# Kernel optimization log

Hardware: AMD Instinct MI355X
Metric: run time of the kernel (lower is better)

The kernel has to match this reference:

```python
import jax, jax.numpy as jnp
import numpy as np

N_NODES = 50000
IN_C = 128
OUT_C = 128
N_EDGES = 1600000
NEG_SLOPE = 0.2
EPS = 1e-16  # matches torch_geometric softmax denominator epsilon


def setup_inputs() -> dict:
    key = jax.random.key(0)
    k1, k2, k3, k4, k5 = jax.random.split(key, 5)
    glorot = 1.0 / np.sqrt(IN_C)
    x = jax.random.normal(k1, (N_NODES, IN_C), dtype=jnp.float32)
    W = jax.random.normal(k2, (IN_C, OUT_C), dtype=jnp.float32) * glorot
    a_src = jax.random.normal(k3, (OUT_C,), dtype=jnp.float32) * glorot
    a_dst = jax.random.normal(k4, (OUT_C,), dtype=jnp.float32) * glorot
    bias = jnp.zeros((OUT_C,), dtype=jnp.float32)
    edge_index = jax.random.randint(k5, (2, N_EDGES), 0, N_NODES, dtype=jnp.int32)
    return {"x": x, "W": W, "a_src": a_src, "a_dst": a_dst,
            "bias": bias, "edge_index": edge_index}


def reference(x, W, a_src, a_dst, bias, edge_index):
    N = x.shape[0]
    # add self loops (GATConv default add_self_loops=True)
    loops = jnp.arange(N, dtype=edge_index.dtype)
    src = jnp.concatenate([edge_index[0], loops])  # [E+N]
    dst = jnp.concatenate([edge_index[1], loops])

    h = x @ W                                      # [N, out]
    alpha_s = h @ a_src                            # [N]
    alpha_d = h @ a_dst                            # [N]

    e = alpha_s[src] + alpha_d[dst]                # [E+N]
    e = jnp.where(e > 0, e, NEG_SLOPE * e)         # leaky_relu

    # neighbor-wise (per destination node) stable softmax
    m = jax.ops.segment_max(e, dst, num_segments=N)
    ex = jnp.exp(e - m[dst])
    denom = jax.ops.segment_sum(ex, dst, num_segments=N)
    alpha = ex / (denom[dst] + EPS)

    # weighted aggregation of source features into destination nodes
    msgs = h[src] * alpha[:, None]                 # [E+N, out]
    out = jax.ops.segment_sum(msgs, dst, num_segments=N) + bias
    return jax.nn.relu(out)
```

## Files before the change

kernel.cpp:

```cpp
#include <hip/hip_runtime.h>
#include <hip/hip_fp16.h>

#define C 128
#define NEG_SLOPE 0.2f
#define SM_EPS 1e-16f
#define BKT_SHIFT 8
#define BKT_MASK 255
#define BIN_CHUNK 8192
#define WP 136

typedef unsigned int uint32;
typedef __attribute__((ext_vector_type(8))) short bf16x8;
typedef __attribute__((ext_vector_type(4))) float f32x4;

static __device__ __forceinline__ unsigned short f2bf(float f) {
    uint32 u = __float_as_uint(f);
    uint32 r = 0x7FFFu + ((u >> 16) & 1u);
    return (unsigned short)((u + r) >> 16);
}
static __device__ __forceinline__ uint32 f2bf2(float lo, float hi) {
    return (uint32)f2bf(lo) | ((uint32)f2bf(hi) << 16);
}
static __device__ __forceinline__ uint32 f2h(float f) {
    __half h = __float2half(f);
    return (uint32)*reinterpret_cast<unsigned short*>(&h);
}
static __device__ __forceinline__ float h2f(uint32 b) {
    unsigned short s = (unsigned short)(b & 0xffffu);
    __half h = *reinterpret_cast<__half*>(&s);
    return __half2float(h);
}

__global__ __launch_bounds__(256) void cvtw_kernel(const float* __restrict__ W,
                                                   uint32* __restrict__ Wf,
                                                   int* __restrict__ bucket_cnt,
                                                   int* __restrict__ bucket_progress, int NB) {
    int gid = blockIdx.x * 256 + threadIdx.x;
    if (blockIdx.x == 0 && threadIdx.x < NB) {
        bucket_cnt[threadIdx.x] = 0;
        bucket_progress[threadIdx.x] = 0;
    }
    int j2   = gid & 3;
    int lane = (gid >> 2) & 63;
    int tile = gid >> 8;
    int t = tile >> 2, kk = tile & 3;
    int n = t * 16 + (lane & 15);
    int k = kk * 32 + (lane >> 4) * 8 + j2 * 2;
    Wf[gid] = f2bf2(W[k * C + n], W[(k + 1) * C + n]);
}

__global__ __launch_bounds__(256) void gemm_hist_kernel(
    const float* __restrict__ x, const uint32* __restrict__ Wf,
    const float* __restrict__ a_src, const float* __restrict__ a_dst,
    unsigned short* __restrict__ hb, float* __restrict__ as_out,
    float* __restrict__ ad_out, int N,
    const int* __restrict__ dst, int* __restrict__ bucket_cnt, int E, int total, int NB)
{
    __shared__ __align__(16) unsigned short slice[4][16 * WP];
    __shared__ int bhist[256];

    const int tid  = threadIdx.x;
    const int lane = tid & 63;
    const int w    = tid >> 6;
    const int row0 = blockIdx.x * 64;
    const int m16  = lane & 15;
    const int q    = lane >> 4;

    bhist[tid] = 0;

    const int row = row0 + w * 16 + m16;
    const bool rv = (row < N);
    const float* xr_p = x + (size_t)(rv ? row : 0) * C + q * 8;

    float4 xr[8];
    #pragma unroll
    for (int kk = 0; kk < 4; ++kk) {
        xr[kk * 2]     = rv ? *(const float4*)(xr_p + kk * 32)     : make_float4(0, 0, 0, 0);
        xr[kk * 2 + 1] = rv ? *(const float4*)(xr_p + kk * 32 + 4) : make_float4(0, 0, 0, 0);
    }

    f32x4 acc[8];
    const f32x4 zz = {0.f, 0.f, 0.f, 0.f};
    #pragma unroll
    for (int t = 0; t < 8; ++t) acc[t] = zz;

    #pragma unroll
    for (int kk = 0; kk < 4; ++kk) {
        union { bf16x8 v; uint32 u[4]; } au;
        float4 p0 = xr[kk * 2], p1 = xr[kk * 2 + 1];
        au.u[0] = f2bf2(p0.x, p0.y); au.u[1] = f2bf2(p0.z, p0.w);
        au.u[2] = f2bf2(p1.x, p1.y); au.u[3] = f2bf2(p1.z, p1.w);
        #pragma unroll
        for (int t = 0; t < 8; ++t) {
            bf16x8 b = *(const bf16x8*)&Wf[((t * 4 + kk) * 64 + lane) * 4];
            acc[t] = __builtin_amdgcn_mfma_f32_16x16x32_bf16(au.v, b, acc[t], 0, 0, 0);
        }
    }

    float ps[4] = {0.f, 0.f, 0.f, 0.f}, pd[4] = {0.f, 0.f, 0.f, 0.f};
    #pragma unroll
    for (int t = 0; t < 8; ++t) {
        float av = a_src[t * 16 + m16];
        float dv = a_dst[t * 16 + m16];
        #pragma unroll
        for (int r = 0; r < 4; ++r) {
            ps[r] += acc[t][r] * av;
            pd[r] += acc[t][r] * dv;
        }
    }
    #pragma unroll
    for (int r = 0; r < 4; ++r) {
        #pragma unroll
        for (int off = 1; off < 16; off <<= 1) {
            ps[r] += __shfl_xor(ps[r], off, 64);
            pd[r] += __shfl_xor(pd[r], off, 64);
        }
    }
    if (m16 == 0) {
        #pragma unroll
        for (int r = 0; r < 4; ++r) {
            int rr = row0 + w * 16 + q * 4 + r;
            if (rr < N) { as_out[rr] = ps[r]; ad_out[rr] = pd[r]; }
        }
    }

    #pragma unroll
    for (int t = 0; t < 8; ++t)
        #pragma unroll
        for (int r = 0; r < 4; ++r)
            slice[w][(q * 4 + r) * WP + t * 16 + m16] = f2bf(acc[t][r]);
    __syncthreads();
    #pragma unroll
    for (int it = 0; it < 4; ++it) {
        int r = it * 4 + q;
        int rr = row0 + w * 16 + r;
        if (rr < N) {
            bf16x8 v = *(const bf16x8*)&slice[w][r * WP + m16 * 8];
            *(bf16x8*)&hb[(size_t)rr * C + m16 * 8] = v;
        }
    }

    for (int i = blockIdx.x * 256 + tid; i < total; i += gridDim.x * 256) {
        int d = (i < E) ? dst[i] : (i - E);
        atomicAdd(&bhist[d >> BKT_SHIFT], 1);
    }
    __syncthreads();
    if (tid < NB && bhist[tid]) atomicAdd(&bucket_cnt[tid], bhist[tid]);
}

__global__ __launch_bounds__(1024) void bin_kernel(
    const int* __restrict__ src, const int* __restrict__ dst,
    const int* __restrict__ bucket_cnt, int* __restrict__ bucket_progress,
    uint32* __restrict__ packed, int E, int total, int NB)
{
    __shared__ uint32 lsrc[BIN_CHUNK];
    __shared__ unsigned short ldst[BIN_CHUNK];
    __shared__ int hist[256];
    __shared__ int base[256];
    __shared__ int boff[256];
    __shared__ int wave_tot[4];
    const int tid = threadIdx.x;
    const int start = blockIdx.x * BIN_CHUNK;
    const int end = min(start + BIN_CHUNK, total);
    const int n = end - start;

    int v = 0, xx = 0;
    if (tid < 256) {
        hist[tid] = 0;
        const int lane = tid & 63;
        v = (tid < NB) ? bucket_cnt[tid] : 0;
        xx = v;
        #pragma unroll
        for (int o = 1; o < 64; o <<= 1) {
            int t = __shfl_up(xx, o, 64);
            if (lane >= o) xx += t;
        }
        if (lane == 63) wave_tot[tid >> 6] = xx;
    }
    for (int i = start + tid; i < end; i += 1024) {
        int s = (i < E) ? src[i] : (i - E);
        int d = (i < E) ? dst[i] : (i - E);
        lsrc[i - start] = (uint32)s;
        ldst[i - start] = (unsigned short)d;
    }
    __syncthreads();
    if (tid < 256) {
        const int wid = tid >> 6;
        int wbase = 0;
        #pragma unroll
        for (int w = 0; w < 4; ++w) wbase += (w < wid) ? wave_tot[w] : 0;
        boff[tid] = wbase + xx - v;
    }
    __syncthreads();
    for (int j = tid; j < n; j += 1024)
        atomicAdd(&hist[ldst[j] >> BKT_SHIFT], 1);
    __syncthreads();
    if (tid < NB) {
        int c = hist[tid];
        base[tid] = boff[tid] + (c ? atomicAdd(&bucket_progress[tid], c) : 0);
    }
    if (tid < 256) hist[tid] = 0;
    __syncthreads();
    for (int j = tid; j < n; j += 1024) {
        int d = ldst[j];
        int b = d >> BKT_SHIFT;
        int pos = base[b] + atomicAdd(&hist[b], 1);
        packed[pos] = (lsrc[j] << BKT_SHIFT) | (uint32)(d & BKT_MASK);
    }
}

__global__ __launch_bounds__(1024) void build_kernel(
    const uint32* __restrict__ packed, const int* __restrict__ bucket_cnt,
    const float* __restrict__ as, const float* __restrict__ ad,
    int* __restrict__ row_start, uint32* __restrict__ csr, int N, int NB, int total)
{
    __shared__ int cnt[256];
    __shared__ int cur[256];
    __shared__ float adl[256];
    __shared__ int boff[256];
    __shared__ int wave_tot[8];
    const int tid = threadIdx.x;
    const int b = blockIdx.x;

    int v = 0, xx = 0;
    if (tid < 256) {
        const int lane = tid & 63;
        v = (tid < NB) ? bucket_cnt[tid] : 0;
        xx = v;
        #pragma unroll
        for (int o = 1; o < 64; o <<= 1) {
            int t = __shfl_up(xx, o, 64);
            if (lane >= o) xx += t;
        }
        if (lane == 63) wave_tot[tid >> 6] = xx;
        cnt[tid] = 0;
        int g = (b << BKT_SHIFT) + tid;
        adl[tid] = (g < N) ? ad[g] : 0.f;
    }
    __syncthreads();
    if (tid < 256) {
        const int wid = tid >> 6;
        int wbase = 0;
        #pragma unroll
        for (int w = 0; w < 4; ++w) wbase += (w < wid) ? wave_tot[w] : 0;
        boff[tid] = wbase + xx - v;
    }
    __syncthreads();
    const int off = boff[b];
    const int end = off + ((b < NB) ? bucket_cnt[b] : 0);
    if (b == 0 && tid == 0) row_start[N] = total;

    for (int j = off + tid; j < end; j += 1024)
        atomicAdd(&cnt[packed[j] & BKT_MASK], 1);
    __syncthreads();

    int v2 = 0, x2 = 0;
    if (tid < 256) {
        const int lane = tid & 63;
        v2 = cnt[tid]; x2 = v2;
        #pragma unroll
        for (int o = 1; o < 64; o <<= 1) {
            int t = __shfl_up(x2, o, 64);
            if (lane >= o) x2 += t;
        }
        if (lane == 63) wave_tot[4 + (tid >> 6)] = x2;
    }
    __syncthreads();
    if (tid < 256) {
        const int wid = tid >> 6;
        int wbase = 0;
        #pragma unroll
        for (int w = 0; w < 4; ++w) wbase += (w < wid) ? wave_tot[4 + w] : 0;
        int excl = wbase + x2 - v2;
        int g = (b << BKT_SHIFT) + tid;
        if (g < N) row_start[g] = off + excl;
        cur[tid] = excl;
    }
    __syncthreads();

    for (int j = off + tid; j < end; j += 1024) {
        uint32 p = packed[j];
        int l = (int)(p & BKT_MASK);
        int s = (int)(p >> BKT_SHIFT);
        float e = as[s] + adl[l];
        e = (e > 0.f) ? e : NEG_SLOPE * e;
        int pos = atomicAdd(&cur[l], 1);
        csr[off + pos] = ((uint32)s << 16) | f2h(e);
    }
}

static __device__ __forceinline__ void gather_node_fw(
    int d, const uint32* __restrict__ csr, const int* __restrict__ row_start,
    const unsigned short* __restrict__ hb, const float* __restrict__ bias,
    float* __restrict__ out, int lane)
{
    const int beg = row_start[d];
    const int deg = row_start[d + 1] - beg;
    const int c2 = lane << 1;
    float a0 = 0.f, a1 = 0.f;
    float m = -INFINITY;
    for (int t = lane; t < deg; t += 64) m = fmaxf(m, h2f(csr[beg + t]));
    #pragma unroll
    for (int off = 32; off > 0; off >>= 1) m = fmaxf(m, __shfl_xor(m, off, 64));
    float ssum = 0.f;
    for (int t = lane; t < deg; t += 64) ssum += __expf(h2f(csr[beg + t]) - m);
    #pragma unroll
    for (int off = 32; off > 0; off >>= 1) ssum += __shfl_xor(ssum, off, 64);
    float inv = 1.f / (ssum + SM_EPS);
    for (int t0 = 0; t0 < deg; t0 += 64) {
        int nc = min(64, deg - t0);
        uint32 ent = (lane < nc) ? csr[beg + t0 + lane] : 0xFC00u;
        float wl = (lane < nc) ? __expf(h2f(ent) - m) * inv : 0.f;
        uint32 bc = (ent & 0xffff0000u) | f2h(wl);
        for (int t = 0; t < nc; ++t) {
            uint32 b0 = (uint32)__shfl((int)bc, t, 64);
            uint32 u0 = *(const uint32*)&hb[(size_t)(b0 >> 16) * C + c2];
            float w0 = h2f(b0);
            a0 += __uint_as_float(u0 << 16) * w0;
            a1 += __uint_as_float(u0 & 0xffff0000u) * w0;
        }
    }
    float2 b2 = *(const float2*)&bias[c2];
    a0 = fmaxf(a0 + b2.x, 0.f);
    a1 = fmaxf(a1 + b2.y, 0.f);
    *(float2*)&out[(size_t)d * C + c2] = make_float2(a0, a1);
}

#define ACC4(r, wgt)                                           \
    {                                                          \
        a0 += __uint_as_float((r).x << 16)         * (wgt);    \
        a1 += __uint_as_float((r).x & 0xffff0000u) * (wgt);    \
        a2 += __uint_as_float((r).y << 16)         * (wgt);    \
        a3 += __uint_as_float((r).y & 0xffff0000u) * (wgt);    \
    }

__global__ __launch_bounds__(256) void gather_kernel(
    const uint32* __restrict__ csr, const int* __restrict__ row_start,
    const unsigned short* __restrict__ hb, const float* __restrict__ bias,
    float* __restrict__ out, int N)
{
    __shared__ __align__(16) uint2 lent[4][2][64];
    const int w    = threadIdx.x >> 6;
    const int lane = threadIdx.x & 63;
    const int half = lane >> 5;
    const int hl   = lane & 31;
    const int pair = blockIdx.x * 4 + w;
    const int d0 = pair * 2;
    if (d0 >= N) return;
    const int d = d0 + half;
    const bool valid = (d < N);

    int beg = 0, deg = 0;
    if (valid) { beg = row_start[d]; deg = row_start[d + 1] - beg; }

    int wdeg = deg;
    #pragma unroll
    for (int off = 32; off > 0; off >>= 1) wdeg = max(wdeg, __shfl_xor(wdeg, off, 64));

    if (wdeg > 64) {
        gather_node_fw(d0, csr, row_start, hb, bias, out, lane);
        if (d0 + 1 < N) gather_node_fw(d0 + 1, csr, row_start, hb, bias, out, lane);
        return;
    }

    uint32 ent0 = (hl < deg) ? csr[beg + hl] : 0xFC00u;
    uint32 ent1 = (32 + hl < deg) ? csr[beg + 32 + hl] : 0xFC00u;
    float e0 = h2f(ent0), e1 = h2f(ent1);
    float m = fmaxf(e0, e1);
    #pragma unroll
    for (int off = 16; off > 0; off >>= 1) m = fmaxf(m, __shfl_xor(m, off, 64));
    float p0 = (hl < deg) ? __expf(e0 - m) : 0.f;
    float p1 = (32 + hl < deg) ? __expf(e1 - m) : 0.f;
    float ssum = p0 + p1;
    #pragma unroll
    for (int off = 16; off > 0; off >>= 1) ssum += __shfl_xor(ssum, off, 64);
    const float inv = 1.f / (ssum + SM_EPS);

    lent[w][half][hl]      = make_uint2((ent0 & 0xffff0000u) >> 8, __float_as_uint(p0 * inv));
    lent[w][half][32 + hl] = make_uint2((ent1 & 0xffff0000u) >> 8, __float_as_uint(p1 * inv));
    __builtin_amdgcn_wave_barrier();

    const uint32 cb = (uint32)(hl << 3);
    const char* hbB = (const char*)hb;
    const uint2* lp = &lent[w][half][0];
    float a0 = 0.f, a1 = 0.f, a2 = 0.f, a3 = 0.f;

    int t = 0;
    for (; t + 8 <= deg; t += 8) {
        uint4 q0 = *(const uint4*)(lp + t);
        uint4 q1 = *(const uint4*)(lp + t + 2);
        uint4 q2 = *(const uint4*)(lp + t + 4);
        uint4 q3 = *(const uint4*)(lp + t + 6);
        uint2 r0 = *(const uint2*)(hbB + (q0.x + cb));
        uint2 r1 = *(const uint2*)(hbB + (q0.z + cb));
        uint2 r2 = *(const uint2*)(hbB + (q1.x + cb));
        uint2 r3 = *(const uint2*)(hbB + (q1.z + cb));
        uint2 r4 = *(const uint2*)(hbB + (q2.x + cb));
        uint2 r5 = *(const uint2*)(hbB + (q2.z + cb));
        uint2 r6 = *(const uint2*)(hbB + (q3.x + cb));
        uint2 r7 = *(const uint2*)(hbB + (q3.z + cb));
        float w0 = __uint_as_float(q0.y), w1 = __uint_as_float(q0.w);
        float w2 = __uint_as_float(q1.y), w3 = __uint_as_float(q1.w);
        float w4 = __uint_as_float(q2.y), w5 = __uint_as_float(q2.w);
        float w6 = __uint_as_float(q3.y), w7 = __uint_as_float(q3.w);
        ACC4(r0, w0) ACC4(r1, w1) ACC4(r2, w2) ACC4(r3, w3)
        ACC4(r4, w4) ACC4(r5, w5) ACC4(r6, w6) ACC4(r7, w7)
    }
    for (; t < deg; ++t) {
        uint2 q = lp[t];
        uint2 r = *(const uint2*)(hbB + (q.x + cb));
        float wt = __uint_as_float(q.y);
        ACC4(r, wt)
    }

    if (valid) {
        const int c4 = hl << 2;
        float4 bb = *(const float4*)&bias[c4];
        float4 o;
        o.x = fmaxf(a0 + bb.x, 0.f);
        o.y = fmaxf(a1 + bb.y, 0.f);
        o.z = fmaxf(a2 + bb.z, 0.f);
        o.w = fmaxf(a3 + bb.w, 0.f);
        *(float4*)&out[(size_t)d * C + c4] = o;
    }
}

extern "C" void kernel_launch(void* const* d_in, const int* in_sizes, int n_in,
                              void* d_out, int out_size, void* d_ws, size_t ws_size,
                              hipStream_t stream) {
    const float* x     = (const float*)d_in[0];
    const float* W     = (const float*)d_in[1];
    const float* a_src = (const float*)d_in[2];
    const float* a_dst = (const float*)d_in[3];
    const float* bias  = (const float*)d_in[4];
    const int*   edge  = (const int*)d_in[5];

    const int N = in_sizes[0] / C;
    const int E = in_sizes[5] / 2;
    const int total = E + N;
    const int* src = edge;
    const int* dst = edge + E;
    float* out = (float*)d_out;

    const int NB = (N + BKT_MASK) >> BKT_SHIFT;

    float* ws = (float*)d_ws;
    unsigned short* hb = (unsigned short*)ws;
    float* as = (float*)(hb + (size_t)N * C);
    float* ad = as + N;
    int* row_start       = (int*)(ad + N);
    uint32* packed       = (uint32*)(row_start + (N + 2));
    uint32* csr          = packed + total;
    uint32* Wf           = csr + total;
    int* bucket_cnt      = (int*)(Wf + 8192);
    int* bucket_progress = bucket_cnt + NB;

    cvtw_kernel<<<32, 256, 0, stream>>>(W, Wf, bucket_cnt, bucket_progress, NB);
    gemm_hist_kernel<<<(N + 63) / 64, 256, 0, stream>>>(
        x, Wf, a_src, a_dst, hb, as, ad, N, dst, bucket_cnt, E, total, NB);
    bin_kernel<<<(total + BIN_CHUNK - 1) / BIN_CHUNK, 1024, 0, stream>>>(
        src, dst, bucket_cnt, bucket_progress, packed, E, total, NB);
    build_kernel<<<NB, 1024, 0, stream>>>(packed, bucket_cnt, as, ad, row_start,
                                          csr, N, NB, total);
    gather_kernel<<<((N + 1) / 2 + 3) / 4, 256, 0, stream>>>(csr, row_start, hb, bias, out, N);
}
```

Before: 203.8 us.

## Replace bucketed two-pass CSR build with per-node atomic count, scan, scatter

Drops the bucket histogram plus bin/build kernels in favour of a per-destination-node degree count done with global atomics in the GEMM kernel, a single-block prefix scan, and an atomic-position scatter that writes the CSR entries directly. This removes the intermediate packed buffer and one full pass over the edges. The costs are contended global atomics on random addresses, a serial single-workgroup scan over 50k nodes, and uncoalesced scattered writes. It also adds a 16-edge unrolled step to the gather loop to keep more loads in flight.

```diff
diff --git a/kernel.cpp b/kernel.cpp
--- a/kernel.cpp
+++ b/kernel.cpp
@@ -4,10 +4,6 @@
 #define C 128
 #define NEG_SLOPE 0.2f
 #define SM_EPS 1e-16f
-#define BKT_SHIFT 8
-#define BKT_MASK 255
-#define BIN_CHUNK 8192
-#define WP 136
 
 typedef unsigned int uint32;
 typedef __attribute__((ext_vector_type(8))) short bf16x8;
@@ -31,15 +27,13 @@
     return __half2float(h);
 }
 
+#define WP 136
+
 __global__ __launch_bounds__(256) void cvtw_kernel(const float* __restrict__ W,
                                                    uint32* __restrict__ Wf,
-                                                   int* __restrict__ bucket_cnt,
-                                                   int* __restrict__ bucket_progress, int NB) {
+                                                   int* __restrict__ cur, int N) {
     int gid = blockIdx.x * 256 + threadIdx.x;
-    if (blockIdx.x == 0 && threadIdx.x < NB) {
-        bucket_cnt[threadIdx.x] = 0;
-        bucket_progress[threadIdx.x] = 0;
-    }
+    for (int i = gid; i < N; i += 8192) cur[i] = 0;
     int j2   = gid & 3;
     int lane = (gid >> 2) & 63;
     int tile = gid >> 8;
@@ -54,10 +48,9 @@
     const float* __restrict__ a_src, const float* __restrict__ a_dst,
     unsigned short* __restrict__ hb, float* __restrict__ as_out,
     float* __restrict__ ad_out, int N,
-    const int* __restrict__ dst, int* __restrict__ bucket_cnt, int E, int total, int NB)
+    const int* __restrict__ dst, int* __restrict__ cur, int E, int total)
 {
     __shared__ __align__(16) unsigned short slice[4][16 * WP];
-    __shared__ int bhist[256];
 
     const int tid  = threadIdx.x;
     const int lane = tid & 63;
@@ -66,8 +59,6 @@
     const int m16  = lane & 15;
     const int q    = lane >> 4;
 
-    bhist[tid] = 0;
-
     const int row = row0 + w * 16 + m16;
     const bool rv = (row < N);
     const float* xr_p = x + (size_t)(rv ? row : 0) * C + q * 8;
@@ -95,6 +86,11 @@
             bf16x8 b = *(const bf16x8*)&Wf[((t * 4 + kk) * 64 + lane) * 4];
             acc[t] = __builtin_amdgcn_mfma_f32_16x16x32_bf16(au.v, b, acc[t], 0, 0, 0);
         }
+    }
+
+    for (int i = blockIdx.x * 256 + tid; i < total; i += gridDim.x * 256) {
+        int d = (i < E) ? dst[i] : (i - E);
+        atomicAdd(&cur[d], 1);
     }
 
     float ps[4] = {0.f, 0.f, 0.f, 0.f}, pd[4] = {0.f, 0.f, 0.f, 0.f};
@@ -139,154 +135,60 @@
             *(bf16x8*)&hb[(size_t)rr * C + m16 * 8] = v;
         }
     }
-
-    for (int i = blockIdx.x * 256 + tid; i < total; i += gridDim.x * 256) {
-        int d = (i < E) ? dst[i] : (i - E);
-        atomicAdd(&bhist[d >> BKT_SHIFT], 1);
-    }
+}
+
+__global__ __launch_bounds__(1024) void scan_kernel(
+    int* __restrict__ cur, int* __restrict__ row_start, int N, int total)
+{
+    __shared__ int wtot[16];
+    __shared__ int carry;
+    const int tid  = threadIdx.x;
+    const int lane = tid & 63;
+    const int wid  = tid >> 6;
+    if (tid == 0) carry = 0;
     __syncthreads();
-    if (tid < NB && bhist[tid]) atomicAdd(&bucket_cnt[tid], bhist[tid]);
-}
-
-__global__ __launch_bounds__(1024) void bin_kernel(
+    const int nstrip = (N + 1023) >> 10;
+    for (int sIdx = 0; sIdx < nstrip; ++sIdx) {
+        int idx = (sIdx << 10) + tid;
+        int v = (idx < N) ? cur[idx] : 0;
+        int x = v;
+        #pragma unroll
+        for (int o = 1; o < 64; o <<= 1) {
+            int t = __shfl_up(x, o, 64);
+            if (lane >= o) x += t;
+        }
+        if (lane == 63) wtot[wid] = x;
+        __syncthreads();
+        int wbase = 0;
+        #pragma unroll
+        for (int w2 = 0; w2 < 16; ++w2) wbase += (w2 < wid) ? wtot[w2] : 0;
+        int excl = carry + wbase + x - v;
+        if (idx < N) { row_start[idx] = excl; cur[idx] = excl; }
+        __syncthreads();
+        if (tid == 0) {
+            int tot = 0;
+            #pragma unroll
+            for (int w2 = 0; w2 < 16; ++w2) tot += wtot[w2];
+            carry += tot;
+        }
+        __syncthreads();
+    }
+    if (tid == 0) row_start[N] = total;
+}
+
+__global__ __launch_bounds__(256) void scatter_kernel(
     const int* __restrict__ src, const int* __restrict__ dst,
-    const int* __restrict__ bucket_cnt, int* __restrict__ bucket_progress,
-    uint32* __restrict__ packed, int E, int total, int NB)
-{
-    __shared__ uint32 lsrc[BIN_CHUNK];
-    __shared__ unsigned short ldst[BIN_CHUNK];
-    __shared__ int hist[256];
-    __shared__ int base[256];
-    __shared__ int boff[256];
-    __shared__ int wave_tot[4];
-    const int tid = threadIdx.x;
-    const int start = blockIdx.x * BIN_CHUNK;
-    const int end = min(start + BIN_CHUNK, total);
-    const int n = end - start;
-
-    int v = 0, xx = 0;
-    if (tid < 256) {
-        hist[tid] = 0;
-        const int lane = tid & 63;
-        v = (tid < NB) ? bucket_cnt[tid] : 0;
-        xx = v;
-        #pragma unroll
-        for (int o = 1; o < 64; o <<= 1) {
-            int t = __shfl_up(xx, o, 64);
-            if (lane >= o) xx += t;
-        }
-        if (lane == 63) wave_tot[tid >> 6] = xx;
-    }
-    for (int i = start + tid; i < end; i += 1024) {
-        int s = (i < E) ? src[i] : (i - E);
-        int d = (i < E) ? dst[i] : (i - E);
-        lsrc[i - start] = (uint32)s;
-        ldst[i - start] = (unsigned short)d;
-    }
-    __syncthreads();
-    if (tid < 256) {
-        const int wid = tid >> 6;
-        int wbase = 0;
-        #pragma unroll
-        for (int w = 0; w < 4; ++w) wbase += (w < wid) ? wave_tot[w] : 0;
-        boff[tid] = wbase + xx - v;
-    }
-    __syncthreads();
-    for (int j = tid; j < n; j += 1024)
-        atomicAdd(&hist[ldst[j] >> BKT_SHIFT], 1);
-    __syncthreads();
-    if (tid < NB) {
-        int c = hist[tid];
-        base[tid] = boff[tid] + (c ? atomicAdd(&bucket_progress[tid], c) : 0);
-    }
-    if (tid < 256) hist[tid] = 0;
-    __syncthreads();
-    for (int j = tid; j < n; j += 1024) {
-        int d = ldst[j];
-        int b = d >> BKT_SHIFT;
-        int pos = base[b] + atomicAdd(&hist[b], 1);
-        packed[pos] = (lsrc[j] << BKT_SHIFT) | (uint32)(d & BKT_MASK);
-    }
-}
-
-__global__ __launch_bounds__(1024) void build_kernel(
-    const uint32* __restrict__ packed, const int* __restrict__ bucket_cnt,
     const float* __restrict__ as, const float* __restrict__ ad,
-    int* __restrict__ row_start, uint32* __restrict__ csr, int N, int NB, int total)
-{
-    __shared__ int cnt[256];
-    __shared__ int cur[256];
-    __shared__ float adl[256];
-    __shared__ int boff[256];
-    __shared__ int wave_tot[8];
-    const int tid = threadIdx.x;
-    const int b = blockIdx.x;
-
-    int v = 0, xx = 0;
-    if (tid < 256) {
-        const int lane = tid & 63;
-        v = (tid < NB) ? bucket_cnt[tid] : 0;
-        xx = v;
-        #pragma unroll
-        for (int o = 1; o < 64; o <<= 1) {
-            int t = __shfl_up(xx, o, 64);
-            if (lane >= o) xx += t;
-        }
-        if (lane == 63) wave_tot[tid >> 6] = xx;
-        cnt[tid] = 0;
-        int g = (b << BKT_SHIFT) + tid;
-        adl[tid] = (g < N) ? ad[g] : 0.f;
-    }
-    __syncthreads();
-    if (tid < 256) {
-        const int wid = tid >> 6;
-        int wbase = 0;
-        #pragma unroll
-        for (int w = 0; w < 4; ++w) wbase += (w < wid) ? wave_tot[w] : 0;
-        boff[tid] = wbase + xx - v;
-    }
-    __syncthreads();
-    const int off = boff[b];
-    const int end = off + ((b < NB) ? bucket_cnt[b] : 0);
-    if (b == 0 && tid == 0) row_start[N] = total;
-
-    for (int j = off + tid; j < end; j += 1024)
-        atomicAdd(&cnt[packed[j] & BKT_MASK], 1);
-    __syncthreads();
-
-    int v2 = 0, x2 = 0;
-    if (tid < 256) {
-        const int lane = tid & 63;
-        v2 = cnt[tid]; x2 = v2;
-        #pragma unroll
-        for (int o = 1; o < 64; o <<= 1) {
-            int t = __shfl_up(x2, o, 64);
-            if (lane >= o) x2 += t;
-        }
-        if (lane == 63) wave_tot[4 + (tid >> 6)] = x2;
-    }
-    __syncthreads();
-    if (tid < 256) {
-        const int wid = tid >> 6;
-        int wbase = 0;
-        #pragma unroll
-        for (int w = 0; w < 4; ++w) wbase += (w < wid) ? wave_tot[4 + w] : 0;
-        int excl = wbase + x2 - v2;
-        int g = (b << BKT_SHIFT) + tid;
-        if (g < N) row_start[g] = off + excl;
-        cur[tid] = excl;
-    }
-    __syncthreads();
-
-    for (int j = off + tid; j < end; j += 1024) {
-        uint32 p = packed[j];
-        int l = (int)(p & BKT_MASK);
-        int s = (int)(p >> BKT_SHIFT);
-        float e = as[s] + adl[l];
-        e = (e > 0.f) ? e : NEG_SLOPE * e;
-        int pos = atomicAdd(&cur[l], 1);
-        csr[off + pos] = ((uint32)s << 16) | f2h(e);
-    }
+    int* __restrict__ cur, uint32* __restrict__ csr, int E, int total)
+{
+    int i = blockIdx.x * 256 + threadIdx.x;
+    if (i >= total) return;
+    int s = (i < E) ? src[i] : (i - E);
+    int d = (i < E) ? dst[i] : (i - E);
+    float e = as[s] + ad[d];
+    e = (e > 0.f) ? e : NEG_SLOPE * e;
+    int pos = atomicAdd(&cur[d], 1);
+    csr[pos] = ((uint32)s << 16) | f2h(e);
 }
 
 static __device__ __forceinline__ void gather_node_fw(
@@ -386,30 +288,44 @@
     float a0 = 0.f, a1 = 0.f, a2 = 0.f, a3 = 0.f;
 
     int t = 0;
+    for (; t + 16 <= deg; t += 16) {
+        uint4 qq[8];
+        #pragma unroll
+        for (int k = 0; k < 8; ++k) qq[k] = *(const uint4*)(lp + t + 2 * k);
+        uint2 rr[16];
+        #pragma unroll
+        for (int k = 0; k < 8; ++k) {
+            rr[2 * k]     = *(const uint2*)(hbB + (qq[k].x + cb));
+            rr[2 * k + 1] = *(const uint2*)(hbB + (qq[k].z + cb));
+        }
+        #pragma unroll
+        for (int k = 0; k < 8; ++k) {
+            float wA = __uint_as_float(qq[k].y), wB = __uint_as_float(qq[k].w);
+            ACC4(rr[2 * k], wA)
+            ACC4(rr[2 * k + 1], wB)
+        }
+    }
     for (; t + 8 <= deg; t += 8) {
-        uint4 q0 = *(const uint4*)(lp + t);
-        uint4 q1 = *(const uint4*)(lp + t + 2);
-        uint4 q2 = *(const uint4*)(lp + t + 4);
-        uint4 q3 = *(const uint4*)(lp + t + 6);
-        uint2 r0 = *(const uint2*)(hbB + (q0.x + cb));
-        uint2 r1 = *(const uint2*)(hbB + (q0.z + cb));
-        uint2 r2 = *(const uint2*)(hbB + (q1.x + cb));
-        uint2 r3 = *(const uint2*)(hbB + (q1.z + cb));
-        uint2 r4 = *(const uint2*)(hbB + (q2.x + cb));
-        uint2 r5 = *(const uint2*)(hbB + (q2.z + cb));
-        uint2 r6 = *(const uint2*)(hbB + (q3.x + cb));
-        uint2 r7 = *(const uint2*)(hbB + (q3.z + cb));
-        float w0 = __uint_as_float(q0.y), w1 = __uint_as_float(q0.w);
-        float w2 = __uint_as_float(q1.y), w3 = __uint_as_float(q1.w);
-        float w4 = __uint_as_float(q2.y), w5 = __uint_as_float(q2.w);
-        float w6 = __uint_as_float(q3.y), w7 = __uint_as_float(q3.w);
-        ACC4(r0, w0) ACC4(r1, w1) ACC4(r2, w2) ACC4(r3, w3)
-        ACC4(r4, w4) ACC4(r5, w5) ACC4(r6, w6) ACC4(r7, w7)
+        uint4 qq[4];
+        #pragma unroll
+        for (int k = 0; k < 4; ++k) qq[k] = *(const uint4*)(lp + t + 2 * k);
+        uint2 rr[8];
+        #pragma unroll
+        for (int k = 0; k < 4; ++k) {
+            rr[2 * k]     = *(const uint2*)(hbB + (qq[k].x + cb));
+            rr[2 * k + 1] = *(const uint2*)(hbB + (qq[k].z + cb));
+        }
+        #pragma unroll
+        for (int k = 0; k < 4; ++k) {
+            float wA = __uint_as_float(qq[k].y), wB = __uint_as_float(qq[k].w);
+            ACC4(rr[2 * k], wA)
+            ACC4(rr[2 * k + 1], wB)
+        }
     }
     for (; t < deg; ++t) {
-        uint2 q = lp[t];
-        uint2 r = *(const uint2*)(hbB + (q.x + cb));
-        float wt = __uint_as_float(q.y);
+        uint2 qv = lp[t];
+        uint2 r = *(const uint2*)(hbB + (qv.x + cb));
+        float wt = __uint_as_float(qv.y);
         ACC4(r, wt)
     }
 
@@ -442,25 +358,20 @@
     const int* dst = edge + E;
     float* out = (float*)d_out;
 
-    const int NB = (N + BKT_MASK) >> BKT_SHIFT;
-
     float* ws = (float*)d_ws;
     unsigned short* hb = (unsigned short*)ws;
     float* as = (float*)(hb + (size_t)N * C);
     float* ad = as + N;
-    int* row_start       = (int*)(ad + N);
-    uint32* packed       = (uint32*)(row_start + (N + 2));
-    uint32* csr          = packed + total;
-    uint32* Wf           = csr + total;
-    int* bucket_cnt      = (int*)(Wf + 8192);
-    int* bucket_progress = bucket_cnt + NB;
-
-    cvtw_kernel<<<32, 256, 0, stream>>>(W, Wf, bucket_cnt, bucket_progress, NB);
+    int* row_start = (int*)(ad + N);
+    int* cur       = row_start + (N + 2);
+    uint32* csr    = (uint32*)(cur + N);
+    uint32* Wf     = csr + total;
+
+    cvtw_kernel<<<32, 256, 0, stream>>>(W, Wf, cur, N);
     gemm_hist_kernel<<<(N + 63) / 64, 256, 0, stream>>>(
-        x, Wf, a_src, a_dst, hb, as, ad, N, dst, bucket_cnt, E, total, NB);
-    bin_kernel<<<(total + BIN_CHUNK - 1) / BIN_CHUNK, 1024, 0, stream>>>(
-        src, dst, bucket_cnt, bucket_progress, packed, E, total, NB);
-    build_kernel<<<NB, 1024, 0, stream>>>(packed, bucket_cnt, as, ad, row_start,
-                                          csr, N, NB, total);
+        x, Wf, a_src, a_dst, hb, as, ad, N, dst, cur, E, total);
+    scan_kernel<<<1, 1024, 0, stream>>>(cur, row_start, N, total);
+    scatter_kernel<<<(total + 255) / 256, 256, 0, stream>>>(
+        src, dst, as, ad, cur, csr, E, total);
     gather_kernel<<<((N + 1) / 2 + 3) / 4, 256, 0, stream>>>(csr, row_start, hb, bias, out, N);
 }
```

Result: slower. 343.8 us (+68.7%).

## Fuse edge histogram into W conversion and binning into GEMM kernel

Applied to the files above, without the earlier changes.

Moves the destination-bucket histogram out of the GEMM kernel and into the weight-conversion kernel, which now runs on 512 blocks. The edge binning pass is merged into the GEMM kernel, with each block handling 2048 edges held in registers instead of 8192 staged through LDS. Counter zeroing is done with a memset. The aim is to drop one kernel launch and let the GEMM work overlap with the scatter into buckets. The cost is a grid sized to the larger of the row count and the chunk count, extra LDS and registers in the fused kernel, and smaller binning chunks that issue more global atomics on the bucket progress counters.

```diff
diff --git a/kernel.cpp b/kernel.cpp
--- a/kernel.cpp
+++ b/kernel.cpp
@@ -6,7 +6,7 @@
 #define SM_EPS 1e-16f
 #define BKT_SHIFT 8
 #define BKT_MASK 255
-#define BIN_CHUNK 8192
+#define GB_CHUNK 2048
 #define WP 136
 
 typedef unsigned int uint32;
@@ -31,33 +31,48 @@
     return __half2float(h);
 }
 
-__global__ __launch_bounds__(256) void cvtw_kernel(const float* __restrict__ W,
-                                                   uint32* __restrict__ Wf,
-                                                   int* __restrict__ bucket_cnt,
-                                                   int* __restrict__ bucket_progress, int NB) {
-    int gid = blockIdx.x * 256 + threadIdx.x;
-    if (blockIdx.x == 0 && threadIdx.x < NB) {
-        bucket_cnt[threadIdx.x] = 0;
-        bucket_progress[threadIdx.x] = 0;
-    }
-    int j2   = gid & 3;
-    int lane = (gid >> 2) & 63;
-    int tile = gid >> 8;
-    int t = tile >> 2, kk = tile & 3;
-    int n = t * 16 + (lane & 15);
-    int k = kk * 32 + (lane >> 4) * 8 + j2 * 2;
-    Wf[gid] = f2bf2(W[k * C + n], W[(k + 1) * C + n]);
-}
-
-__global__ __launch_bounds__(256) void gemm_hist_kernel(
+__global__ __launch_bounds__(256) void cvtw_hist_kernel(
+    const float* __restrict__ W, uint32* __restrict__ Wf,
+    const int* __restrict__ dst, int* __restrict__ bucket_cnt,
+    int E, int total, int NB)
+{
+    __shared__ int bhist[256];
+    const int tid = threadIdx.x;
+    bhist[tid] = 0;
+    const int gid = blockIdx.x * 256 + tid;
+    if (gid < 8192) {
+        int j2   = gid & 3;
+        int lane = (gid >> 2) & 63;
+        int tile = gid >> 8;
+        int t = tile >> 2, kk = tile & 3;
+        int n = t * 16 + (lane & 15);
+        int k = kk * 32 + (lane >> 4) * 8 + j2 * 2;
+        Wf[gid] = f2bf2(W[k * C + n], W[(k + 1) * C + n]);
+    }
+    __syncthreads();
+    const int stride = gridDim.x * 256;
+    for (int i = gid; i < total; i += stride) {
+        int d = (i < E) ? dst[i] : (i - E);
+        atomicAdd(&bhist[d >> BKT_SHIFT], 1);
+    }
+    __syncthreads();
+    if (tid < NB && bhist[tid]) atomicAdd(&bucket_cnt[tid], bhist[tid]);
+}
+
+__global__ __launch_bounds__(256) void gemm_bin_kernel(
     const float* __restrict__ x, const uint32* __restrict__ Wf,
     const float* __restrict__ a_src, const float* __restrict__ a_dst,
     unsigned short* __restrict__ hb, float* __restrict__ as_out,
     float* __restrict__ ad_out, int N,
-    const int* __restrict__ dst, int* __restrict__ bucket_cnt, int E, int total, int NB)
+    const int* __restrict__ src, const int* __restrict__ dst,
+    const int* __restrict__ bucket_cnt, int* __restrict__ bucket_progress,
+    uint32* __restrict__ packed, int E, int total, int NB)
 {
     __shared__ __align__(16) unsigned short slice[4][16 * WP];
-    __shared__ int bhist[256];
+    __shared__ int hist[256];
+    __shared__ int base[256];
+    __shared__ int boff[256];
+    __shared__ int wave_tot[4];
 
     const int tid  = threadIdx.x;
     const int lane = tid & 63;
@@ -66,146 +81,127 @@
     const int m16  = lane & 15;
     const int q    = lane >> 4;
 
-    bhist[tid] = 0;
-
-    const int row = row0 + w * 16 + m16;
-    const bool rv = (row < N);
-    const float* xr_p = x + (size_t)(rv ? row : 0) * C + q * 8;
-
-    float4 xr[8];
-    #pragma unroll
-    for (int kk = 0; kk < 4; ++kk) {
-        xr[kk * 2]     = rv ? *(const float4*)(xr_p + kk * 32)     : make_float4(0, 0, 0, 0);
-        xr[kk * 2 + 1] = rv ? *(const float4*)(xr_p + kk * 32 + 4) : make_float4(0, 0, 0, 0);
-    }
-
-    f32x4 acc[8];
-    const f32x4 zz = {0.f, 0.f, 0.f, 0.f};
-    #pragma unroll
-    for (int t = 0; t < 8; ++t) acc[t] = zz;
-
-    #pragma unroll
-    for (int kk = 0; kk < 4; ++kk) {
-        union { bf16x8 v; uint32 u[4]; } au;
-        float4 p0 = xr[kk * 2], p1 = xr[kk * 2 + 1];
-        au.u[0] = f2bf2(p0.x, p0.y); au.u[1] = f2bf2(p0.z, p0.w);
-        au.u[2] = f2bf2(p1.x, p1.y); au.u[3] = f2bf2(p1.z, p1.w);
+    if (row0 < N) {
+        const int row = row0 + w * 16 + m16;
+        const bool rv = (row < N);
+        const float* xr_p = x + (size_t)(rv ? row : 0) * C + q * 8;
+
+        float4 xr[8];
+        #pragma unroll
+        for (int kk = 0; kk < 4; ++kk) {
+            xr[kk * 2]     = rv ? *(const float4*)(xr_p + kk * 32)     : make_float4(0, 0, 0, 0);
+            xr[kk * 2 + 1] = rv ? *(const float4*)(xr_p + kk * 32 + 4) : make_float4(0, 0, 0, 0);
+        }
+
+        f32x4 acc[8];
+        const f32x4 zz = {0.f, 0.f, 0.f, 0.f};
+        #pragma unroll
+        for (int t = 0; t < 8; ++t) acc[t] = zz;
+
+        #pragma unroll
+        for (int kk = 0; kk < 4; ++kk) {
+            union { bf16x8 v; uint32 u[4]; } au;
+            float4 p0 = xr[kk * 2], p1 = xr[kk * 2 + 1];
+            au.u[0] = f2bf2(p0.x, p0.y); au.u[1] = f2bf2(p0.z, p0.w);
+            au.u[2] = f2bf2(p1.x, p1.y); au.u[3] = f2bf2(p1.z, p1.w);
+            #pragma unroll
+            for (int t = 0; t < 8; ++t) {
+                bf16x8 b = *(const bf16x8*)&Wf[((t * 4 + kk) * 64 + lane) * 4];
+                acc[t] = __builtin_amdgcn_mfma_f32_16x16x32_bf16(au.v, b, acc[t], 0, 0, 0);
+            }
+        }
+
+        float ps[4] = {0.f, 0.f, 0.f, 0.f}, pd[4] = {0.f, 0.f, 0.f, 0.f};
         #pragma unroll
         for (int t = 0; t < 8; ++t) {
-            bf16x8 b = *(const bf16x8*)&Wf[((t * 4 + kk) * 64 + lane) * 4];
-            acc[t] = __builtin_amdgcn_mfma_f32_16x16x32_bf16(au.v, b, acc[t], 0, 0, 0);
-        }
-    }
-
-    float ps[4] = {0.f, 0.f, 0.f, 0.f}, pd[4] = {0.f, 0.f, 0.f, 0.f};
-    #pragma unroll
-    for (int t = 0; t < 8; ++t) {
-        float av = a_src[t * 16 + m16];
-        float dv = a_dst[t * 16 + m16];
+            float av = a_src[t * 16 + m16];
+            float dv = a_dst[t * 16 + m16];
+            #pragma unroll
+            for (int r = 0; r < 4; ++r) {
+                ps[r] += acc[t][r] * av;
+                pd[r] += acc[t][r] * dv;
+            }
+        }
         #pragma unroll
         for (int r = 0; r < 4; ++r) {
-            ps[r] += acc[t][r] * av;
-            pd[r] += acc[t][r] * dv;
-        }
-    }
-    #pragma unroll
-    for (int r = 0; r < 4; ++r) {
-        #pragma unroll
-        for (int off = 1; off < 16; off <<= 1) {
-            ps[r] += __shfl_xor(ps[r], off, 64);
-            pd[r] += __shfl_xor(pd[r], off, 64);
-        }
-    }
-    if (m16 == 0) {
-        #pragma unroll
-        for (int r = 0; r < 4; ++r) {
-            int rr = row0 + w * 16 + q * 4 + r;
-            if (rr < N) { as_out[rr] = ps[r]; ad_out[rr] = pd[r]; }
-        }
-    }
-
-    #pragma unroll
-    for (int t = 0; t < 8; ++t)
-        #pragma unroll
-        for (int r = 0; r < 4; ++r)
-            slice[w][(q * 4 + r) * WP + t * 16 + m16] = f2bf(acc[t][r]);
-    __syncthreads();
-    #pragma unroll
-    for (int it = 0; it < 4; ++it) {
-        int r = it * 4 + q;
-        int rr = row0 + w * 16 + r;
-        if (rr < N) {
-            bf16x8 v = *(const bf16x8*)&slice[w][r * WP + m16 * 8];
-            *(bf16x8*)&hb[(size_t)rr * C + m16 * 8] = v;
-        }
-    }
-
-    for (int i = blockIdx.x * 256 + tid; i < total; i += gridDim.x * 256) {
-        int d = (i < E) ? dst[i] : (i - E);
-        atomicAdd(&bhist[d >> BKT_SHIFT], 1);
-    }
-    __syncthreads();
-    if (tid < NB && bhist[tid]) atomicAdd(&bucket_cnt[tid], bhist[tid]);
-}
-
-__global__ __launch_bounds__(1024) void bin_kernel(
-    const int* __restrict__ src, const int* __restrict__ dst,
-    const int* __restrict__ bucket_cnt, int* __restrict__ bucket_progress,
-    uint32* __restrict__ packed, int E, int total, int NB)
-{
-    __shared__ uint32 lsrc[BIN_CHUNK];
-    __shared__ unsigned short ldst[BIN_CHUNK];
-    __shared__ int hist[256];
-    __shared__ int base[256];
-    __shared__ int boff[256];
-    __shared__ int wave_tot[4];
-    const int tid = threadIdx.x;
-    const int start = blockIdx.x * BIN_CHUNK;
-    const int end = min(start + BIN_CHUNK, total);
-    const int n = end - start;
-
-    int v = 0, xx = 0;
-    if (tid < 256) {
-        hist[tid] = 0;
-        const int lane = tid & 63;
-        v = (tid < NB) ? bucket_cnt[tid] : 0;
-        xx = v;
-        #pragma unroll
-        for (int o = 1; o < 64; o <<= 1) {
-            int t = __shfl_up(xx, o, 64);
-            if (lane >= o) xx += t;
-        }
-        if (lane == 63) wave_tot[tid >> 6] = xx;
-    }
-    for (int i = start + tid; i < end; i += 1024) {
-        int s = (i < E) ? src[i] : (i - E);
-        int d = (i < E) ? dst[i] : (i - E);
-        lsrc[i - start] = (uint32)s;
-        ldst[i - start] = (unsigned short)d;
-    }
-    __syncthreads();
-    if (tid < 256) {
-        const int wid = tid >> 6;
+            #pragma unroll
+            for (int off = 1; off < 16; off <<= 1) {
+                ps[r] += __shfl_xor(ps[r], off, 64);
+                pd[r] += __shfl_xor(pd[r], off, 64);
+            }
+        }
+        if (m16 == 0) {
+            #pragma unroll
+            for (int r = 0; r < 4; ++r) {
+                int rr = row0 + w * 16 + q * 4 + r;
+                if (rr < N) { as_out[rr] = ps[r]; ad_out[rr] = pd[r]; }
+            }
+        }
+
+        #pragma unroll
+        for (int t = 0; t < 8; ++t)
+            #pragma unroll
+            for (int r = 0; r < 4; ++r)
+                slice[w][(q * 4 + r) * WP + t * 16 + m16] = f2bf(acc[t][r]);
+        __syncthreads();
+        #pragma unroll
+        for (int it = 0; it < 4; ++it) {
+            int r = it * 4 + q;
+            int rr = row0 + w * 16 + r;
+            if (rr < N) {
+                bf16x8 v = *(const bf16x8*)&slice[w][r * WP + m16 * 8];
+                *(bf16x8*)&hb[(size_t)rr * C + m16 * 8] = v;
+            }
+        }
+    }
+
+    const int start = blockIdx.x * GB_CHUNK;
+    if (start >= total) return;
+    const int end = min(start + GB_CHUNK, total);
+
+    hist[tid] = 0;
+    int v = (tid < NB) ? bucket_cnt[tid] : 0;
+    int xx = v;
+    #pragma unroll
+    for (int o = 1; o < 64; o <<= 1) {
+        int t = __shfl_up(xx, o, 64);
+        if (lane >= o) xx += t;
+    }
+    if (lane == 63) wave_tot[w] = xx;
+    __syncthreads();
+    {
         int wbase = 0;
         #pragma unroll
-        for (int w = 0; w < 4; ++w) wbase += (w < wid) ? wave_tot[w] : 0;
+        for (int w2 = 0; w2 < 4; ++w2) wbase += (w2 < w) ? wave_tot[w2] : 0;
         boff[tid] = wbase + xx - v;
     }
-    __syncthreads();
-    for (int j = tid; j < n; j += 1024)
-        atomicAdd(&hist[ldst[j] >> BKT_SHIFT], 1);
+
+    int es[8], ed[8];
+    #pragma unroll
+    for (int k = 0; k < 8; ++k) {
+        int i = start + k * 256 + tid;
+        if (i < end) {
+            es[k] = (i < E) ? src[i] : (i - E);
+            ed[k] = (i < E) ? dst[i] : (i - E);
+        } else ed[k] = -1;
+    }
+    #pragma unroll
+    for (int k = 0; k < 8; ++k)
+        if (ed[k] >= 0) atomicAdd(&hist[ed[k] >> BKT_SHIFT], 1);
     __syncthreads();
     if (tid < NB) {
         int c = hist[tid];
         base[tid] = boff[tid] + (c ? atomicAdd(&bucket_progress[tid], c) : 0);
     }
-    if (tid < 256) hist[tid] = 0;
-    __syncthreads();
-    for (int j = tid; j < n; j += 1024) {
-        int d = ldst[j];
-        int b = d >> BKT_SHIFT;
-        int pos = base[b] + atomicAdd(&hist[b], 1);
-        packed[pos] = (lsrc[j] << BKT_SHIFT) | (uint32)(d & BKT_MASK);
+    hist[tid] = 0;
+    __syncthreads();
+    #pragma unroll
+    for (int k = 0; k < 8; ++k) {
+        if (ed[k] >= 0) {
+            int b = ed[k] >> BKT_SHIFT;
+            int pos = base[b] + atomicAdd(&hist[b], 1);
+            packed[pos] = ((uint32)es[k] << BKT_SHIFT) | (uint32)(ed[k] & BKT_MASK);
+        }
     }
 }
 
@@ -455,11 +451,15 @@
     int* bucket_cnt      = (int*)(Wf + 8192);
     int* bucket_progress = bucket_cnt + NB;
 
-    cvtw_kernel<<<32, 256, 0, stream>>>(W, Wf, bucket_cnt, bucket_progress, NB);
-    gemm_hist_kernel<<<(N + 63) / 64, 256, 0, stream>>>(
-        x, Wf, a_src, a_dst, hb, as, ad, N, dst, bucket_cnt, E, total, NB);
-    bin_kernel<<<(total + BIN_CHUNK - 1) / BIN_CHUNK, 1024, 0, stream>>>(
-        src, dst, bucket_cnt, bucket_progress, packed, E, total, NB);
+    const int nrow   = (N + 63) / 64;
+    const int nchunk = (total + GB_CHUNK - 1) / GB_CHUNK;
+    const int grid2  = (nrow > nchunk) ? nrow : nchunk;
+
+    hipMemsetAsync(bucket_cnt, 0, (size_t)(2 * NB) * sizeof(int), stream);
+    cvtw_hist_kernel<<<512, 256, 0, stream>>>(W, Wf, dst, bucket_cnt, E, total, NB);
+    gemm_bin_kernel<<<grid2, 256, 0, stream>>>(
+        x, Wf, a_src, a_dst, hb, as, ad, N, src, dst,
+        bucket_cnt, bucket_progress, packed, E, total, NB);
     build_kernel<<<NB, 1024, 0, stream>>>(packed, bucket_cnt, as, ad, row_start,
                                           csr, N, NB, total);
     gather_kernel<<<((N + 1) / 2 + 3) / 4, 256, 0, stream>>>(csr, row_start, hb, bias, out, N);
```

Result: slower. 207.9 us (+2.0%).
